# Kernel optimization log

Measured on AMD Instinct MI355X. Metric: run time of the kernel, lower is better.

Reference implementation:

```python
import jax, jax.numpy as jnp
import numpy as np

N, E = 50000, 800000          # nodes, edges (avg degree 16)
NFEAT, NHID, NCLASS = 256, 128, 64
HEADS = 4
P_DROP = 0.5


def setup_inputs() -> dict:
    key = jax.random.key(0)
    ks = jax.random.split(key, 12)

    def w(k, shape, fan_in):
        return jax.random.normal(k, shape, jnp.float32) * (1.0 / np.sqrt(fan_in))

    return {
        "features": jax.random.normal(ks[0], (N, NFEAT), jnp.float32),
        "src": jax.random.randint(ks[1], (E,), 0, N, jnp.int32),
        "dst": jax.random.randint(ks[2], (E,), 0, N, jnp.int32),
        # gc1: nfeat->nhid, 3 layers
        "wqkv1_0": w(ks[3], (3, NFEAT, NHID), NFEAT),
        "wqkv1_r": w(ks[4], (2, 3, NHID, NHID), NHID),
        "wo1": w(ks[5], (3, NHID, NHID), NHID),
        # gc2: nhid->nclass, 3 layers
        "wqkv2_0": w(ks[6], (3, NHID, NCLASS), NHID),
        "wqkv2_r": w(ks[7], (2, 3, NCLASS, NCLASS), NCLASS),
        "wo2": w(ks[8], (3, NCLASS, NCLASS), NCLASS),
        # gc3: nhid->nclass, 3 layers
        "wqkv3_0": w(ks[9], (3, NHID, NCLASS), NHID),
        "wqkv3_r": w(ks[10], (2, 3, NCLASS, NCLASS), NCLASS),
        "wo3": w(ks[11], (3, NCLASS, NCLASS), NCLASS),
    }


def _l2norm(x):
    # F.normalize(x): L2 along dim 1, eps=1e-12
    n = jnp.sqrt(jnp.sum(x * x, axis=1, keepdims=True))
    return x / jnp.maximum(n, 1e-12)


def _graph_transformer(h, src, dst, wqkv0, wqkvr, wo):
    """Stacked graph-transformer layers: gather q[dst]/k[src], edge-softmax per dst, scatter-sum v."""
    n = h.shape[0]
    n_layers = wo.shape[0]
    for l in range(n_layers):  # fixed small structural loop
        w = wqkv0 if l == 0 else wqkvr[l - 1]
        out_dim = w.shape[2]
        dh = out_dim // HEADS
        q = (h @ w[0]).reshape(n, HEADS, dh)
        k = (h @ w[1]).reshape(n, HEADS, dh)
        v = (h @ w[2]).reshape(n, HEADS, dh)
        # per-edge attention scores [E, H]
        s = jnp.einsum('ehd,ehd->eh', q[dst], k[src]) / np.sqrt(dh).astype(np.float32)
        # edge softmax over incoming edges of each dst node
        m = jax.ops.segment_max(s, dst, num_segments=n)
        e = jnp.exp(s - m[dst])
        denom = jax.ops.segment_sum(e, dst, num_segments=n)
        alpha = e / denom[dst]
        agg = jax.ops.segment_sum(alpha[:, :, None] * v[src], dst, num_segments=n)
        h = agg.reshape(n, out_dim) @ wo[l]
        if l < n_layers - 1:
            h = jax.nn.relu(h)
    return h


def reference(features, src, dst, wqkv1_0, wqkv1_r, wo1,
              wqkv2_0, wqkv2_r, wo2, wqkv3_0, wqkv3_r, wo3):
    key = jax.random.key(42)
    kd, ke = jax.random.split(key)

    x = _graph_transformer(features, src, dst, wqkv1_0, wqkv1_r, wo1)
    x = jax.nn.relu(_l2norm(x))
    # dropout (training=True), deterministic key
    keep = jax.random.bernoulli(kd, 1.0 - P_DROP, x.shape)
    x = jnp.where(keep, x / (1.0 - P_DROP), 0.0)

    mu = _l2norm(_graph_transformer(x, src, dst, wqkv2_0, wqkv2_r, wo2))
    logvar = _l2norm(_graph_transformer(x, src, dst, wqkv3_0, wqkv3_r, wo3))

    # reparameterize (training): std = exp(logvar) + 1e-12 (matches source exactly)
    std = jnp.exp(logvar) + 1e-12
    eps = jax.random.normal(ke, std.shape, std.dtype)
    z = eps * std + mu
    return z
```

## Files before the change

kernel.cpp:

```cpp
#include <hip/hip_runtime.h>
#include <stdint.h>
#include <math.h>

#define NN 50000
#define NE 800000
#define NH 4

typedef __attribute__((ext_vector_type(8))) short short8;
typedef __attribute__((ext_vector_type(4))) float floatx4;

__device__ inline float bf2f(uint32_t u16)
{
    return __uint_as_float(u16 << 16);
}
__device__ inline uint16_t f2bf(float f)
{
    uint32_t u = __float_as_uint(f);
    uint32_t r = (u + 0x7fffu + ((u >> 16) & 1u)) >> 16;
    return (uint16_t)r;
}
__device__ inline void unpk8(uint4 u, float* f)
{
    f[0] = bf2f(u.x & 0xffffu); f[1] = bf2f(u.x >> 16);
    f[2] = bf2f(u.y & 0xffffu); f[3] = bf2f(u.y >> 16);
    f[4] = bf2f(u.z & 0xffffu); f[5] = bf2f(u.z >> 16);
    f[6] = bf2f(u.w & 0xffffu); f[7] = bf2f(u.w >> 16);
}

__host__ __device__ inline void tf2x32(uint32_t k0, uint32_t k1,
                                       uint32_t x0, uint32_t x1,
                                       uint32_t& o0, uint32_t& o1)
{
    uint32_t ks2 = k0 ^ k1 ^ 0x1BD11BDAu;
    x0 += k0; x1 += k1;
#define TF_R(r) { x0 += x1; x1 = (x1 << (r)) | (x1 >> (32 - (r))); x1 ^= x0; }
    TF_R(13) TF_R(15) TF_R(26) TF_R(6)
    x0 += k1;  x1 += ks2 + 1u;
    TF_R(17) TF_R(29) TF_R(16) TF_R(24)
    x0 += ks2; x1 += k0 + 2u;
    TF_R(13) TF_R(15) TF_R(26) TF_R(6)
    x0 += k0;  x1 += k1 + 3u;
    TF_R(17) TF_R(29) TF_R(16) TF_R(24)
    x0 += k1;  x1 += ks2 + 4u;
    TF_R(13) TF_R(15) TF_R(26) TF_R(6)
    x0 += ks2; x1 += k0 + 5u;
#undef TF_R
    o0 = x0; o1 = x1;
}

__device__ inline uint32_t jax_bits32(uint32_t k0, uint32_t k1, uint32_t idx)
{
    uint32_t a, b;
    tf2x32(k0, k1, 0u, idx, a, b);
    return a ^ b;
}

__device__ inline float jax_u01(uint32_t bits)
{
    return __uint_as_float((bits >> 9) | 0x3f800000u) - 1.0f;
}

__device__ inline float erfinv_f(float x)
{
    float w = -log1pf(-x * x);
    float p;
    if (w < 5.0f) {
        w = w - 2.5f;
        p = 2.81022636e-08f;
        p = fmaf(p, w, 3.43273939e-07f);
        p = fmaf(p, w, -3.5233877e-06f);
        p = fmaf(p, w, -4.39150654e-06f);
        p = fmaf(p, w, 0.00021858087f);
        p = fmaf(p, w, -0.00125372503f);
        p = fmaf(p, w, -0.00417768164f);
        p = fmaf(p, w, 0.246640727f);
        p = fmaf(p, w, 1.50140941f);
    } else {
        w = sqrtf(w) - 3.0f;
        p = -0.000200214257f;
        p = fmaf(p, w, 0.000100950558f);
        p = fmaf(p, w, 0.00134934322f);
        p = fmaf(p, w, -0.00367342844f);
        p = fmaf(p, w, 0.00573950773f);
        p = fmaf(p, w, -0.0076224613f);
        p = fmaf(p, w, 0.00943887047f);
        p = fmaf(p, w, 1.00167406f);
        p = fmaf(p, w, 2.83297682f);
    }
    return p * x;
}

__global__ __launch_bounds__(256) void fill_u32_k(uint32_t* p, uint32_t v, int n)
{
    int i = blockIdx.x * blockDim.x + threadIdx.x;
    if (i < n) p[i] = v;
}

__global__ __launch_bounds__(256) void f2bf_vec_k(const float* __restrict__ in,
                                                  uint16_t* __restrict__ out, int n)
{
    int i = (blockIdx.x * blockDim.x + threadIdx.x) * 4;
    if (i >= n) return;
    float4 v = *(const float4*)(in + i);
    out[i + 0] = f2bf(v.x); out[i + 1] = f2bf(v.y);
    out[i + 2] = f2bf(v.z); out[i + 3] = f2bf(v.w);
}

struct WSeg { const float* src; int B, K, C, off; };
struct WSegs { WSeg s[18]; };

__global__ __launch_bounds__(256) void wconv_k(WSegs segs, uint16_t* __restrict__ Wt)
{
    WSeg sg = segs.s[blockIdx.y];
    int n = sg.B * sg.K * sg.C;
    int i = blockIdx.x * 256 + threadIdx.x;
    if (i >= n) return;
    int kc = sg.K * sg.C;
    int b = i / kc;
    int rr = i - b * kc;
    int k = rr / sg.C;
    int c = rr - k * sg.C;
    Wt[(size_t)sg.off + (size_t)(b * sg.C + c) * sg.K + k] = f2bf(sg.src[i]);
}

__global__ __launch_bounds__(256) void hist_k(const int* __restrict__ dst, int* __restrict__ deg)
{
    int e = blockIdx.x * blockDim.x + threadIdx.x;
    if (e < NE) atomicAdd(&deg[dst[e]], 1);
}

#define SCAN_CHUNK 1024
#define SCAN_NBLK  ((NN + SCAN_CHUNK - 1) / SCAN_CHUNK)

__global__ __launch_bounds__(256) void scan1_k(const int* __restrict__ deg,
                                               int* __restrict__ rowptr,
                                               int* __restrict__ bsums)
{
    __shared__ int lds[256];
    int b = blockIdx.x, t = threadIdx.x;
    int base = b * SCAN_CHUNK + t * 4;
    int v0 = (base + 0 < NN) ? deg[base + 0] : 0;
    int v1 = (base + 1 < NN) ? deg[base + 1] : 0;
    int v2 = (base + 2 < NN) ? deg[base + 2] : 0;
    int v3 = (base + 3 < NN) ? deg[base + 3] : 0;
    int s = v0 + v1 + v2 + v3;
    lds[t] = s;
    __syncthreads();
    for (int off = 1; off < 256; off <<= 1) {
        int x = (t >= off) ? lds[t - off] : 0;
        __syncthreads();
        lds[t] += x;
        __syncthreads();
    }
    int excl = lds[t] - s;
    if (base + 0 < NN) rowptr[base + 0] = excl;
    if (base + 1 < NN) rowptr[base + 1] = excl + v0;
    if (base + 2 < NN) rowptr[base + 2] = excl + v0 + v1;
    if (base + 3 < NN) rowptr[base + 3] = excl + v0 + v1 + v2;
    if (t == 255) bsums[b] = lds[255];
}

__global__ void scan2_k(int* bsums)
{
    if (threadIdx.x == 0 && blockIdx.x == 0) {
        int run = 0;
        for (int i = 0; i < SCAN_NBLK; i++) { int t = bsums[i]; bsums[i] = run; run += t; }
    }
}

__global__ __launch_bounds__(256) void scan3_k(int* __restrict__ rowptr,
                                               const int* __restrict__ bsums,
                                               int* __restrict__ cursor)
{
    int i = blockIdx.x * blockDim.x + threadIdx.x;
    if (i < NN) {
        int r = rowptr[i] + bsums[i / SCAN_CHUNK];
        rowptr[i] = r;
        cursor[i] = r;
    }
    if (i == 0) rowptr[NN] = NE;
}

__global__ __launch_bounds__(256) void csr_scatter_k(const int* __restrict__ src,
                                                     const int* __restrict__ dst,
                                                     int* __restrict__ cursor,
                                                     int* __restrict__ esrc)
{
    int e = blockIdx.x * blockDim.x + threadIdx.x;
    if (e >= NE) return;
    int d = dst[e];
    int pos = atomicAdd(&cursor[d], 1);
    esrc[pos] = src[e];
}

template<int K, int CH>
__global__ __launch_bounds__(256) void gemm_mfma_k(const uint16_t* __restrict__ A,
                                                   const uint16_t* __restrict__ Wt,
                                                   uint16_t* __restrict__ C,
                                                   int Ntot, int relu)
{
    constexpr int KP = K + 8;
    constexpr int KC = K / 8;
    constexpr int NT = CH / 16;
    extern __shared__ uint16_t smem[];
    uint16_t* As = smem;
    uint16_t* Ws = smem + 64 * KP;

    const int tid = threadIdx.x;
    const int row0 = blockIdx.x * 64;
    const int w  = tid >> 6;
    const int l  = tid & 63;
    const int lm = l & 15;
    const int lq = l >> 4;

    for (int i = tid; i < 64 * KC; i += 256) {
        int r = i / KC, c = i - r * KC;
        int gr = row0 + r; if (gr >= NN) gr = NN - 1;
        uint4 vv = *(const uint4*)(A + (size_t)gr * K + c * 8);
        *(uint4*)(As + r * KP + c * 8) = vv;
    }

    const uint16_t* a_base = As + (16 * w + lm) * KP + lq * 8;
    const uint16_t* b_base = Ws + lm * KP + lq * 8;

    const int nchunks = Ntot / CH;
    for (int ch = 0; ch < nchunks; ch++) {
        __syncthreads();
        for (int i = tid; i < CH * KC; i += 256) {
            int r = i / KC, c = i - r * KC;
            uint4 vv = *(const uint4*)(Wt + (size_t)(ch * CH + r) * K + c * 8);
            *(uint4*)(Ws + r * KP + c * 8) = vv;
        }
        __syncthreads();

        floatx4 acc[NT];
#pragma unroll
        for (int nt = 0; nt < NT; nt++) acc[nt] = (floatx4){0.f, 0.f, 0.f, 0.f};

#pragma unroll
        for (int ks = 0; ks < K / 32; ks++) {
            short8 av = *(const short8*)(a_base + ks * 32);
#pragma unroll
            for (int nt = 0; nt < NT; nt++) {
                short8 bv = *(const short8*)(b_base + nt * 16 * KP + ks * 32);
                acc[nt] = __builtin_amdgcn_mfma_f32_16x16x32_bf16(av, bv, acc[nt], 0, 0, 0);
            }
        }

        const int rbase = row0 + 16 * w + lq * 4;
        const int cbase = ch * CH + lm;
#pragma unroll
        for (int nt = 0; nt < NT; nt++) {
#pragma unroll
            for (int r = 0; r < 4; r++) {
                int gr = rbase + r;
                if (gr < NN) {
                    float v = acc[nt][r];
                    if (relu) v = fmaxf(v, 0.0f);
                    C[(size_t)gr * Ntot + cbase + nt * 16] = f2bf(v);
                }
            }
        }
    }
}

template<int DH>
__global__ __launch_bounds__(64) void attn_wave_k(const uint16_t* __restrict__ qkv,
                                                  const int* __restrict__ rowptr,
                                                  const int* __restrict__ esrc,
                                                  uint16_t* __restrict__ agg,
                                                  float scale)
{
    constexpr int OD  = NH * DH;
    constexpr int STR = 3 * OD;
    constexpr int QU  = DH / 8;
    constexpr int F2  = OD / 64;
    constexpr int CAP = 128;

    __shared__ float s_sc[NH][CAP + 1];
    __shared__ int   s_sn[CAP];
    __shared__ float s_hdr[2 * NH];

    const int n    = blockIdx.x;
    const int lane = threadIdx.x;
    const int h1   = lane & 3;
    const int e    = lane >> 2;
    const int h2   = lane >> 4;
    const int d0   = (lane & 15) * F2;

    float qf[DH];
    {
        const uint4* qp = (const uint4*)(qkv + (size_t)n * STR + h1 * DH);
#pragma unroll
        for (int i = 0; i < QU; i++) { uint4 u = qp[i]; unpk8(u, &qf[i * 8]); }
    }

    float m = -INFINITY, l = 0.0f;
    float acc[F2];
#pragma unroll
    for (int i = 0; i < F2; i++) acc[i] = 0.0f;

    const int j0 = rowptr[n], j1 = rowptr[n + 1];
    const int voff = 2 * OD + h2 * DH + d0;

    for (int c0 = j0; c0 < j1; c0 += CAP) {
        const int cn = min(j1 - c0, CAP);

        if (lane < cn)      s_sn[lane]      = esrc[c0 + lane];
        if (lane + 64 < cn) s_sn[lane + 64] = esrc[c0 + lane + 64];
        __syncthreads();

        float lm = -INFINITY;
        for (int j = e; j < cn; j += 16) {
            const int sn = s_sn[j];
            const uint4* kp = (const uint4*)(qkv + (size_t)sn * STR + OD + h1 * DH);
            float s = 0.0f;
#pragma unroll
            for (int i = 0; i < QU; i++) {
                uint4 u = kp[i];
                float kf[8];
                unpk8(u, kf);
                s = fmaf(qf[i * 8 + 0], kf[0], s); s = fmaf(qf[i * 8 + 1], kf[1], s);
                s = fmaf(qf[i * 8 + 2], kf[2], s); s = fmaf(qf[i * 8 + 3], kf[3], s);
                s = fmaf(qf[i * 8 + 4], kf[4], s); s = fmaf(qf[i * 8 + 5], kf[5], s);
                s = fmaf(qf[i * 8 + 6], kf[6], s); s = fmaf(qf[i * 8 + 7], kf[7], s);
            }
            s *= scale;
            s_sc[h1][j] = s;
            lm = fmaxf(lm, s);
        }
#pragma unroll
        for (int msk = 4; msk <= 32; msk <<= 1) lm = fmaxf(lm, __shfl_xor(lm, msk, 64));
        const float mn = fmaxf(m, lm);
        const float corr = expf(m - mn);
        m = mn;

        float ls = 0.0f;
        for (int j = e; j < cn; j += 16) {
            float p = expf(s_sc[h1][j] - mn);
            s_sc[h1][j] = p;
            ls += p;
        }
#pragma unroll
        for (int msk = 4; msk <= 32; msk <<= 1) ls += __shfl_xor(ls, msk, 64);
        l = l * corr + ls;
        s_hdr[h1] = corr;
        __syncthreads();

        const float c2 = s_hdr[h2];
#pragma unroll
        for (int i = 0; i < F2; i++) acc[i] *= c2;

        int j = 0;
        for (; j + 4 <= cn; j += 4) {
            int sa = s_sn[j], sb = s_sn[j + 1], sc = s_sn[j + 2], sd = s_sn[j + 3];
            float aa = s_sc[h2][j],     ab = s_sc[h2][j + 1];
            float ac = s_sc[h2][j + 2], ad = s_sc[h2][j + 3];
            if (F2 == 2) {
                uint32_t va = *(const uint32_t*)(qkv + (size_t)sa * STR + voff);
                uint32_t vb = *(const uint32_t*)(qkv + (size_t)sb * STR + voff);
                uint32_t vc = *(const uint32_t*)(qkv + (size_t)sc * STR + voff);
                uint32_t vd = *(const uint32_t*)(qkv + (size_t)sd * STR + voff);
                acc[0] = fmaf(aa, bf2f(va & 0xffffu), acc[0]); acc[1] = fmaf(aa, bf2f(va >> 16), acc[1]);
                acc[0] = fmaf(ab, bf2f(vb & 0xffffu), acc[0]); acc[1] = fmaf(ab, bf2f(vb >> 16), acc[1]);
                acc[0] = fmaf(ac, bf2f(vc & 0xffffu), acc[0]); acc[1] = fmaf(ac, bf2f(vc >> 16), acc[1]);
                acc[0] = fmaf(ad, bf2f(vd & 0xffffu), acc[0]); acc[1] = fmaf(ad, bf2f(vd >> 16), acc[1]);
            } else {
                acc[0] = fmaf(aa, bf2f(qkv[(size_t)sa * STR + voff]), acc[0]);
                acc[0] = fmaf(ab, bf2f(qkv[(size_t)sb * STR + voff]), acc[0]);
                acc[0] = fmaf(ac, bf2f(qkv[(size_t)sc * STR + voff]), acc[0]);
                acc[0] = fmaf(ad, bf2f(qkv[(size_t)sd * STR + voff]), acc[0]);
            }
        }
        for (; j < cn; j++) {
            int sa = s_sn[j];
            float aa = s_sc[h2][j];
            if (F2 == 2) {
                uint32_t va = *(const uint32_t*)(qkv + (size_t)sa * STR + voff);
                acc[0] = fmaf(aa, bf2f(va & 0xffffu), acc[0]); acc[1] = fmaf(aa, bf2f(va >> 16), acc[1]);
            } else {
                acc[0] = fmaf(aa, bf2f(qkv[(size_t)sa * STR + voff]), acc[0]);
            }
        }
        __syncthreads();
    }

    s_hdr[NH + h1] = l;
    __syncthreads();
    const float lf = s_hdr[NH + h2];
    const float inv = (lf > 0.0f) ? 1.0f / lf : 0.0f;
    uint16_t* op = agg + (size_t)n * OD + h2 * DH + d0;
    op[0] = f2bf(acc[0] * inv);
    if (F2 == 2) op[1] = f2bf(acc[1] * inv);
}

__global__ __launch_bounds__(256) void norm_relu_drop_k(const uint16_t* __restrict__ in,
                                                        uint16_t* __restrict__ out,
                                                        uint32_t k0, uint32_t k1)
{
    int row = blockIdx.x * 4 + (threadIdx.x >> 6);
    int lane = threadIdx.x & 63;
    if (row >= NN) return;
    const uint16_t* r = in + (size_t)row * 128;
    float a = bf2f(r[lane]), b = bf2f(r[lane + 64]);
    float ss = fmaf(a, a, b * b);
#pragma unroll
    for (int m = 32; m > 0; m >>= 1) ss += __shfl_xor(ss, m, 64);
    float d = fmaxf(sqrtf(ss), 1e-12f);
    float ya = fmaxf(a / d, 0.0f);
    float yb = fmaxf(b / d, 0.0f);
    uint32_t ia = (uint32_t)row * 128u + (uint32_t)lane;
    float ua = jax_u01(jax_bits32(k0, k1, ia));
    float ub = jax_u01(jax_bits32(k0, k1, ia + 64u));
    uint16_t* o = out + (size_t)row * 128;
    o[lane]      = f2bf((ua < 0.5f) ? ya * 2.0f : 0.0f);
    o[lane + 64] = f2bf((ub < 0.5f) ? yb * 2.0f : 0.0f);
}

__global__ __launch_bounds__(256) void norm64_k(const uint16_t* __restrict__ in,
                                                float* __restrict__ out)
{
    int row = blockIdx.x * 4 + (threadIdx.x >> 6);
    int lane = threadIdx.x & 63;
    if (row >= NN) return;
    float a = bf2f(in[(size_t)row * 64 + lane]);
    float ss = a * a;
#pragma unroll
    for (int m = 32; m > 0; m >>= 1) ss += __shfl_xor(ss, m, 64);
    float d = fmaxf(sqrtf(ss), 1e-12f);
    out[(size_t)row * 64 + lane] = a / d;
}

__global__ __launch_bounds__(256) void final_z_k(const float* __restrict__ mu,
                                                 const float* __restrict__ lv,
                                                 float* __restrict__ out,
                                                 uint32_t k0, uint32_t k1)
{
    int i = blockIdx.x * blockDim.x + threadIdx.x;
    if (i >= NN * 64) return;
    const float LO = -0.99999994f;
    float u01 = jax_u01(jax_bits32(k0, k1, (uint32_t)i));
    float u = fmaxf(LO, fmaf(u01, 2.0f, LO));
    float eps = 1.41421354f * erfinv_f(u);
    float stdv = expf(lv[i]) + 1e-12f;
    out[i] = fmaf(eps, stdv, mu[i]);
}

struct Bufs {
    uint16_t* Wt;
    uint16_t* feat_bf;
    uint16_t* qkv;
    uint16_t* agg;
    uint16_t* h1;
    uint16_t* h2;
    uint16_t* x;
    float* mu;
    float* lv;
    int* rowptr;
    int* cursor;
    int* bsums;
    int* esrc;
};

static void gemm_launch(int K, const uint16_t* A, const uint16_t* Wt, uint16_t* C,
                        int Ntot, int relu, hipStream_t s)
{
    int grid = (NN + 63) / 64;
    switch (K) {
    case 256: {
        size_t lds = (size_t)(64 + 32) * (256 + 8) * 2;
        gemm_mfma_k<256, 32><<<grid, 256, lds, s>>>(A, Wt, C, Ntot, relu);
        break;
    }
    case 128: {
        size_t lds = (size_t)(64 + 64) * (128 + 8) * 2;
        gemm_mfma_k<128, 64><<<grid, 256, lds, s>>>(A, Wt, C, Ntot, relu);
        break;
    }
    default: {
        size_t lds = (size_t)(64 + 64) * (64 + 8) * 2;
        gemm_mfma_k<64, 64><<<grid, 256, lds, s>>>(A, Wt, C, Ntot, relu);
        break;
    }
    }
}

static void run_gt_layer(const uint16_t* h_in, int K, int od,
                         const uint16_t* wqkv_t, const uint16_t* wo_t, bool relu,
                         uint16_t* h_out, const Bufs& B, hipStream_t stream)
{
    const int dh = od / NH;
    const float scale = 1.0f / sqrtf((float)dh);

    gemm_launch(K, h_in, wqkv_t, B.qkv, 3 * od, 0, stream);

    if (dh == 32)
        attn_wave_k<32><<<NN, 64, 0, stream>>>(B.qkv, B.rowptr, B.esrc, B.agg, scale);
    else
        attn_wave_k<16><<<NN, 64, 0, stream>>>(B.qkv, B.rowptr, B.esrc, B.agg, scale);

    gemm_launch(od, B.agg, wo_t, h_out, od, relu ? 1 : 0, stream);
}

extern "C" void kernel_launch(void* const* d_in, const int* in_sizes, int n_in,
                              void* d_out, int out_size, void* d_ws, size_t ws_size,
                              hipStream_t stream)
{
    const float* feat    = (const float*)d_in[0];
    const int*   src     = (const int*)d_in[1];
    const int*   dst     = (const int*)d_in[2];
    const float* wqkv1_0 = (const float*)d_in[3];
    const float* wqkv1_r = (const float*)d_in[4];
    const float* wo1     = (const float*)d_in[5];
    const float* wqkv2_0 = (const float*)d_in[6];
    const float* wqkv2_r = (const float*)d_in[7];
    const float* wo2     = (const float*)d_in[8];
    const float* wqkv3_0 = (const float*)d_in[9];
    const float* wqkv3_r = (const float*)d_in[10];
    const float* wo3     = (const float*)d_in[11];
    float* out = (float*)d_out;

    char* wp = (char*)d_ws;
    auto alloc = [&](size_t bytes) { char* p = wp; wp += (bytes + 255) & ~(size_t)255; return p; };

    WSegs segs;
    int offs[18];
    int acc_off = 0;
    auto seg = [&](int i, const float* p, int Bc, int Kc, int Cc) {
        segs.s[i].src = p; segs.s[i].B = Bc; segs.s[i].K = Kc; segs.s[i].C = Cc;
        segs.s[i].off = acc_off; offs[i] = acc_off; acc_off += Bc * Kc * Cc;
    };
    seg(0,  wqkv1_0,                 3, 256, 128);
    seg(1,  wqkv1_r,                 3, 128, 128);
    seg(2,  wqkv1_r + 3 * 128 * 128, 3, 128, 128);
    seg(3,  wo1,                     1, 128, 128);
    seg(4,  wo1 + 128 * 128,         1, 128, 128);
    seg(5,  wo1 + 2 * 128 * 128,     1, 128, 128);
    seg(6,  wqkv2_0,                 3, 128, 64);
    seg(7,  wqkv2_r,                 3, 64, 64);
    seg(8,  wqkv2_r + 3 * 64 * 64,   3, 64, 64);
    seg(9,  wo2,                     1, 64, 64);
    seg(10, wo2 + 64 * 64,           1, 64, 64);
    seg(11, wo2 + 2 * 64 * 64,       1, 64, 64);
    seg(12, wqkv3_0,                 3, 128, 64);
    seg(13, wqkv3_r,                 3, 64, 64);
    seg(14, wqkv3_r + 3 * 64 * 64,   3, 64, 64);
    seg(15, wo3,                     1, 64, 64);
    seg(16, wo3 + 64 * 64,           1, 64, 64);
    seg(17, wo3 + 2 * 64 * 64,       1, 64, 64);

    Bufs B;
    B.Wt      = (uint16_t*)alloc((size_t)acc_off * 2);
    B.feat_bf = (uint16_t*)alloc((size_t)NN * 256 * 2);
    B.qkv     = (uint16_t*)alloc((size_t)NN * 384 * 2);
    B.agg     = (uint16_t*)alloc((size_t)NN * 128 * 2);
    B.h1      = (uint16_t*)alloc((size_t)NN * 128 * 2);
    B.h2      = (uint16_t*)alloc((size_t)NN * 128 * 2);
    B.x       = (uint16_t*)alloc((size_t)NN * 128 * 2);
    B.mu      = (float*)alloc((size_t)NN * 64 * 4);
    B.lv      = (float*)alloc((size_t)NN * 64 * 4);
    B.rowptr  = (int*)alloc((size_t)(NN + 1) * 4);
    B.cursor  = (int*)alloc((size_t)NN * 4);
    B.bsums   = (int*)alloc((size_t)SCAN_NBLK * 4);
    B.esrc    = (int*)alloc((size_t)NE * 4);

    wconv_k<<<dim3(384, 18), 256, 0, stream>>>(segs, B.Wt);
    f2bf_vec_k<<<(NN * 256 / 4 + 255) / 256, 256, 0, stream>>>(feat, B.feat_bf, NN * 256);

    fill_u32_k<<<(NN + 255) / 256, 256, 0, stream>>>((uint32_t*)B.cursor, 0u, NN);
    hist_k<<<(NE + 255) / 256, 256, 0, stream>>>(dst, B.cursor);
    scan1_k<<<SCAN_NBLK, 256, 0, stream>>>(B.cursor, B.rowptr, B.bsums);
    scan2_k<<<1, 64, 0, stream>>>(B.bsums);
    scan3_k<<<(NN + 255) / 256, 256, 0, stream>>>(B.rowptr, B.bsums, B.cursor);
    csr_scatter_k<<<(NE + 255) / 256, 256, 0, stream>>>(src, dst, B.cursor, B.esrc);

    uint32_t kd0, kd1, ke0, ke1;
    tf2x32(0u, 42u, 0u, 0u, kd0, kd1);
    tf2x32(0u, 42u, 0u, 1u, ke0, ke1);

    run_gt_layer(B.feat_bf, 256, 128, B.Wt + offs[0], B.Wt + offs[3], true,  B.h1, B, stream);
    run_gt_layer(B.h1,      128, 128, B.Wt + offs[1], B.Wt + offs[4], true,  B.h2, B, stream);
    run_gt_layer(B.h2,      128, 128, B.Wt + offs[2], B.Wt + offs[5], false, B.h1, B, stream);

    norm_relu_drop_k<<<NN / 4, 256, 0, stream>>>(B.h1, B.x, kd0, kd1);

    run_gt_layer(B.x,  128, 64, B.Wt + offs[6], B.Wt + offs[9],  true,  B.h1, B, stream);
    run_gt_layer(B.h1, 64,  64, B.Wt + offs[7], B.Wt + offs[10], true,  B.h2, B, stream);
    run_gt_layer(B.h2, 64,  64, B.Wt + offs[8], B.Wt + offs[11], false, B.h1, B, stream);
    norm64_k<<<NN / 4, 256, 0, stream>>>(B.h1, B.mu);

    run_gt_layer(B.x,  128, 64, B.Wt + offs[12], B.Wt + offs[15], true,  B.h1, B, stream);
    run_gt_layer(B.h1, 64,  64, B.Wt + offs[13], B.Wt + offs[16], true,  B.h2, B, stream);
    run_gt_layer(B.h2, 64,  64, B.Wt + offs[14], B.Wt + offs[17], false, B.h1, B, stream);
    norm64_k<<<NN / 4, 256, 0, stream>>>(B.h1, B.lv);

    final_z_k<<<(NN * 64 + 255) / 256, 256, 0, stream>>>(B.mu, B.lv, out, ke0, ke1);
}
```

Before: 865.0 us.

## Pack four nodes per attention block and vectorize V gathers across edge groups

The attention kernel now handles four destination nodes per 256-thread block, one wavefront each, rather than one node per 64-thread block. Scores are kept in registers with a smaller 64-edge chunk. The V aggregation splits lanes into four edge groups, each doing a wide vector load per edge, with a shuffle reduction at the end and packed vector stores. This targets launch overhead, narrow scalar V loads and serialized per-edge work, at the cost of block-wide syncs: every wave in a block must iterate to the maximum chunk count of the four nodes.

```diff
diff --git a/kernel.cpp b/kernel.cpp
--- a/kernel.cpp
+++ b/kernel.cpp
@@ -265,28 +265,32 @@
 }
 
 template<int DH>
-__global__ __launch_bounds__(64) void attn_wave_k(const uint16_t* __restrict__ qkv,
-                                                  const int* __restrict__ rowptr,
-                                                  const int* __restrict__ esrc,
-                                                  uint16_t* __restrict__ agg,
-                                                  float scale)
+__global__ __launch_bounds__(256) void attn_wave_k(const uint16_t* __restrict__ qkv,
+                                                   const int* __restrict__ rowptr,
+                                                   const int* __restrict__ esrc,
+                                                   uint16_t* __restrict__ agg,
+                                                   float scale)
 {
     constexpr int OD  = NH * DH;
     constexpr int STR = 3 * OD;
     constexpr int QU  = DH / 8;
-    constexpr int F2  = OD / 64;
-    constexpr int CAP = 128;
-
-    __shared__ float s_sc[NH][CAP + 1];
-    __shared__ int   s_sn[CAP];
-    __shared__ float s_hdr[2 * NH];
-
-    const int n    = blockIdx.x;
-    const int lane = threadIdx.x;
+    constexpr int CAP = 64;
+    constexpr int NP  = CAP / 16;
+    constexpr int FV  = OD / 16;
+
+    __shared__ float s_sc[4][CAP][4];
+    __shared__ int   s_sn[4][CAP];
+    __shared__ float s_hdr[4][8];
+    __shared__ int   s_mx[4];
+
+    const int wv   = threadIdx.x >> 6;
+    const int lane = threadIdx.x & 63;
+    const int n    = blockIdx.x * 4 + wv;
     const int h1   = lane & 3;
     const int e    = lane >> 2;
-    const int h2   = lane >> 4;
-    const int d0   = (lane & 15) * F2;
+    const int g    = lane >> 4;
+    const int dl   = lane & 15;
+    const int h2   = dl >> 2;
 
     float qf[DH];
     {
@@ -295,103 +299,120 @@
         for (int i = 0; i < QU; i++) { uint4 u = qp[i]; unpk8(u, &qf[i * 8]); }
     }
 
+    const int j0 = rowptr[n], j1 = rowptr[n + 1];
+    if (lane == 0) s_mx[wv] = (j1 - j0 + CAP - 1) / CAP;
+    __syncthreads();
+    const int cmax = max(max(s_mx[0], s_mx[1]), max(s_mx[2], s_mx[3]));
+
     float m = -INFINITY, l = 0.0f;
-    float acc[F2];
-#pragma unroll
-    for (int i = 0; i < F2; i++) acc[i] = 0.0f;
-
-    const int j0 = rowptr[n], j1 = rowptr[n + 1];
-    const int voff = 2 * OD + h2 * DH + d0;
-
-    for (int c0 = j0; c0 < j1; c0 += CAP) {
-        const int cn = min(j1 - c0, CAP);
-
-        if (lane < cn)      s_sn[lane]      = esrc[c0 + lane];
-        if (lane + 64 < cn) s_sn[lane + 64] = esrc[c0 + lane + 64];
+    float acc[FV];
+#pragma unroll
+    for (int i = 0; i < FV; i++) acc[i] = 0.0f;
+
+    const int voff = 2 * OD + dl * FV;
+
+    for (int ch = 0; ch < cmax; ch++) {
+        const int c0 = j0 + ch * CAP;
+        const int cn = min(max(j1 - c0, 0), CAP);
+
+        if (lane < cn) s_sn[wv][lane] = esrc[c0 + lane];
         __syncthreads();
 
+        float sc[NP];
         float lm = -INFINITY;
-        for (int j = e; j < cn; j += 16) {
-            const int sn = s_sn[j];
-            const uint4* kp = (const uint4*)(qkv + (size_t)sn * STR + OD + h1 * DH);
-            float s = 0.0f;
-#pragma unroll
-            for (int i = 0; i < QU; i++) {
-                uint4 u = kp[i];
-                float kf[8];
-                unpk8(u, kf);
-                s = fmaf(qf[i * 8 + 0], kf[0], s); s = fmaf(qf[i * 8 + 1], kf[1], s);
-                s = fmaf(qf[i * 8 + 2], kf[2], s); s = fmaf(qf[i * 8 + 3], kf[3], s);
-                s = fmaf(qf[i * 8 + 4], kf[4], s); s = fmaf(qf[i * 8 + 5], kf[5], s);
-                s = fmaf(qf[i * 8 + 6], kf[6], s); s = fmaf(qf[i * 8 + 7], kf[7], s);
+#pragma unroll
+        for (int t = 0; t < NP; t++) {
+            const int j = e + 16 * t;
+            float s = -INFINITY;
+            if (j < cn) {
+                const int sn = s_sn[wv][j];
+                const uint4* kp = (const uint4*)(qkv + (size_t)sn * STR + OD + h1 * DH);
+                s = 0.0f;
+#pragma unroll
+                for (int i = 0; i < QU; i++) {
+                    uint4 u = kp[i];
+                    float kf[8];
+                    unpk8(u, kf);
+                    s = fmaf(qf[i * 8 + 0], kf[0], s); s = fmaf(qf[i * 8 + 1], kf[1], s);
+                    s = fmaf(qf[i * 8 + 2], kf[2], s); s = fmaf(qf[i * 8 + 3], kf[3], s);
+                    s = fmaf(qf[i * 8 + 4], kf[4], s); s = fmaf(qf[i * 8 + 5], kf[5], s);
+                    s = fmaf(qf[i * 8 + 6], kf[6], s); s = fmaf(qf[i * 8 + 7], kf[7], s);
+                }
+                s *= scale;
             }
-            s *= scale;
-            s_sc[h1][j] = s;
+            sc[t] = s;
             lm = fmaxf(lm, s);
         }
 #pragma unroll
         for (int msk = 4; msk <= 32; msk <<= 1) lm = fmaxf(lm, __shfl_xor(lm, msk, 64));
         const float mn = fmaxf(m, lm);
-        const float corr = expf(m - mn);
+        const float corr = (m == mn) ? 1.0f : expf(m - mn);
         m = mn;
 
         float ls = 0.0f;
-        for (int j = e; j < cn; j += 16) {
-            float p = expf(s_sc[h1][j] - mn);
-            s_sc[h1][j] = p;
-            ls += p;
+#pragma unroll
+        for (int t = 0; t < NP; t++) {
+            const int j = e + 16 * t;
+            if (j < cn) {
+                float p = expf(sc[t] - mn);
+                s_sc[wv][j][h1] = p;
+                ls += p;
+            }
         }
 #pragma unroll
         for (int msk = 4; msk <= 32; msk <<= 1) ls += __shfl_xor(ls, msk, 64);
         l = l * corr + ls;
-        s_hdr[h1] = corr;
+        if (e == 0) s_hdr[wv][h1] = corr;
         __syncthreads();
 
-        const float c2 = s_hdr[h2];
-#pragma unroll
-        for (int i = 0; i < F2; i++) acc[i] *= c2;
-
-        int j = 0;
-        for (; j + 4 <= cn; j += 4) {
-            int sa = s_sn[j], sb = s_sn[j + 1], sc = s_sn[j + 2], sd = s_sn[j + 3];
-            float aa = s_sc[h2][j],     ab = s_sc[h2][j + 1];
-            float ac = s_sc[h2][j + 2], ad = s_sc[h2][j + 3];
-            if (F2 == 2) {
-                uint32_t va = *(const uint32_t*)(qkv + (size_t)sa * STR + voff);
-                uint32_t vb = *(const uint32_t*)(qkv + (size_t)sb * STR + voff);
-                uint32_t vc = *(const uint32_t*)(qkv + (size_t)sc * STR + voff);
-                uint32_t vd = *(const uint32_t*)(qkv + (size_t)sd * STR + voff);
-                acc[0] = fmaf(aa, bf2f(va & 0xffffu), acc[0]); acc[1] = fmaf(aa, bf2f(va >> 16), acc[1]);
-                acc[0] = fmaf(ab, bf2f(vb & 0xffffu), acc[0]); acc[1] = fmaf(ab, bf2f(vb >> 16), acc[1]);
-                acc[0] = fmaf(ac, bf2f(vc & 0xffffu), acc[0]); acc[1] = fmaf(ac, bf2f(vc >> 16), acc[1]);
-                acc[0] = fmaf(ad, bf2f(vd & 0xffffu), acc[0]); acc[1] = fmaf(ad, bf2f(vd >> 16), acc[1]);
-            } else {
-                acc[0] = fmaf(aa, bf2f(qkv[(size_t)sa * STR + voff]), acc[0]);
-                acc[0] = fmaf(ab, bf2f(qkv[(size_t)sb * STR + voff]), acc[0]);
-                acc[0] = fmaf(ac, bf2f(qkv[(size_t)sc * STR + voff]), acc[0]);
-                acc[0] = fmaf(ad, bf2f(qkv[(size_t)sd * STR + voff]), acc[0]);
-            }
-        }
-        for (; j < cn; j++) {
-            int sa = s_sn[j];
-            float aa = s_sc[h2][j];
-            if (F2 == 2) {
-                uint32_t va = *(const uint32_t*)(qkv + (size_t)sa * STR + voff);
-                acc[0] = fmaf(aa, bf2f(va & 0xffffu), acc[0]); acc[1] = fmaf(aa, bf2f(va >> 16), acc[1]);
-            } else {
-                acc[0] = fmaf(aa, bf2f(qkv[(size_t)sa * STR + voff]), acc[0]);
+        const float c2 = s_hdr[wv][h2];
+#pragma unroll
+        for (int i = 0; i < FV; i++) acc[i] *= c2;
+
+        for (int jb = 0; jb < cn; jb += 4) {
+            const int j = jb + g;
+            if (j < cn) {
+                const float alpha = s_sc[wv][j][h2];
+                const int sn = s_sn[wv][j];
+                if constexpr (FV == 8) {
+                    uint4 u = *(const uint4*)(qkv + (size_t)sn * STR + voff);
+                    float vf[8];
+                    unpk8(u, vf);
+#pragma unroll
+                    for (int i = 0; i < 8; i++) acc[i] = fmaf(alpha, vf[i], acc[i]);
+                } else {
+                    uint2 u = *(const uint2*)(qkv + (size_t)sn * STR + voff);
+                    acc[0] = fmaf(alpha, bf2f(u.x & 0xffffu), acc[0]);
+                    acc[1] = fmaf(alpha, bf2f(u.x >> 16),     acc[1]);
+                    acc[2] = fmaf(alpha, bf2f(u.y & 0xffffu), acc[2]);
+                    acc[3] = fmaf(alpha, bf2f(u.y >> 16),     acc[3]);
+                }
             }
         }
         __syncthreads();
     }
 
-    s_hdr[NH + h1] = l;
+    if (e == 0) s_hdr[wv][4 + h1] = l;
     __syncthreads();
-    const float lf = s_hdr[NH + h2];
+    const float lf = s_hdr[wv][4 + h2];
     const float inv = (lf > 0.0f) ? 1.0f / lf : 0.0f;
-    uint16_t* op = agg + (size_t)n * OD + h2 * DH + d0;
-    op[0] = f2bf(acc[0] * inv);
-    if (F2 == 2) op[1] = f2bf(acc[1] * inv);
+#pragma unroll
+    for (int i = 0; i < FV; i++) {
+        acc[i] += __shfl_xor(acc[i], 16, 64);
+        acc[i] += __shfl_xor(acc[i], 32, 64);
+    }
+    if (g == 0) {
+        uint16_t* op = agg + (size_t)n * OD + dl * FV;
+        uint32_t wword[FV / 2];
+#pragma unroll
+        for (int i = 0; i < FV / 2; i++)
+            wword[i] = (uint32_t)f2bf(acc[2 * i] * inv) | ((uint32_t)f2bf(acc[2 * i + 1] * inv) << 16);
+        if constexpr (FV == 8) {
+            *(uint4*)op = make_uint4(wword[0], wword[1], wword[2], wword[3]);
+        } else {
+            *(uint2*)op = make_uint2(wword[0], wword[1]);
+        }
+    }
 }
 
 __global__ __launch_bounds__(256) void norm_relu_drop_k(const uint16_t* __restrict__ in,
@@ -495,9 +516,9 @@
     gemm_launch(K, h_in, wqkv_t, B.qkv, 3 * od, 0, stream);
 
     if (dh == 32)
-        attn_wave_k<32><<<NN, 64, 0, stream>>>(B.qkv, B.rowptr, B.esrc, B.agg, scale);
+        attn_wave_k<32><<<NN / 4, 256, 0, stream>>>(B.qkv, B.rowptr, B.esrc, B.agg, scale);
     else
-        attn_wave_k<16><<<NN, 64, 0, stream>>>(B.qkv, B.rowptr, B.esrc, B.agg, scale);
+        attn_wave_k<16><<<NN / 4, 256, 0, stream>>>(B.qkv, B.rowptr, B.esrc, B.agg, scale);
 
     gemm_launch(od, B.agg, wo_t, h_out, od, relu ? 1 : 0, stream);
 }
```

New measurement: 1.035 ms. 19.6% more time.
